# Kernel tuning notes

Measured on AMD Instinct MI355X. Metric: run time of the kernel, lower is better.

Reference implementation:

```python
import jax, jax.numpy as jnp
import numpy as np

B, N, DIN, D, E, STEP = 4, 1024, 256, 256, 5, 5


def setup_inputs() -> dict:
    key = jax.random.key(0)
    ks = jax.random.split(key, 14)
    s = 0.02  # weight init scale
    inp = {
        "node_features": jax.random.normal(ks[0], (B, N, DIN), dtype=jnp.float32),
        # dense per-edge-type adjacency; scaled so messages stay in a sane range
        "adj_matrices": jax.random.uniform(ks[1], (B, E, N, N), dtype=jnp.float32) * (2.0 / N),
        "fc_in_w": jax.random.normal(ks[2], (D, DIN), dtype=jnp.float32) * s,
        "fc_in_b": jnp.zeros((D,), dtype=jnp.float32),
        "edge_w": jax.random.normal(ks[3], (E, D, D), dtype=jnp.float32) * s,
        "edge_b": jax.random.normal(ks[4], (E, D), dtype=jnp.float32) * s,
        "gru_w_ih": jax.random.normal(ks[5], (3 * D, D), dtype=jnp.float32) * s,
        "gru_w_hh": jax.random.normal(ks[6], (3 * D, D), dtype=jnp.float32) * s,
        "gru_b_ih": jnp.zeros((3 * D,), dtype=jnp.float32),
        "gru_b_hh": jnp.zeros((3 * D,), dtype=jnp.float32),
        "conv1_w": jax.random.normal(ks[7], (D, D), dtype=jnp.float32) * s,
        "conv1_b": jnp.zeros((D,), dtype=jnp.float32),
        "conv2_w": jax.random.normal(ks[8], (D, D), dtype=jnp.float32) * s,
        "conv2_b": jnp.zeros((D,), dtype=jnp.float32),
    }
    return inp


def _gru_cell(x, h, w_ih, w_hh, b_ih, b_hh):
    # torch GRUCell: gates ordered [r, z, n]
    gi = x @ w_ih.T + b_ih  # [B*N, 3D]
    gh = h @ w_hh.T + b_hh
    ir, iz, inn = jnp.split(gi, 3, axis=-1)
    hr, hz, hn = jnp.split(gh, 3, axis=-1)
    r = jax.nn.sigmoid(ir + hr)
    z = jax.nn.sigmoid(iz + hz)
    n = jnp.tanh(inn + r * hn)
    return (1.0 - z) * n + z * h


def reference(node_features, adj_matrices, fc_in_w, fc_in_b, edge_w, edge_b,
              gru_w_ih, gru_w_hh, gru_b_ih, gru_b_hh,
              conv1_w, conv1_b, conv2_w, conv2_b):
    h = node_features @ fc_in_w.T + fc_in_b  # [B, N, D]
    sum_edge_b = jnp.sum(edge_b, axis=0)  # accumulated biases over edge types
    for _ in range(STEP):
        # messages per edge type: adj_e @ h  -> [B, E, N, D]
        msgs = jnp.einsum('benm,bmd->bend', adj_matrices, h)
        # per-edge-type linear (y = x @ W_e.T) then accumulate over edge types
        acc = jnp.einsum('bend,ekd->bnk', msgs, edge_w) + sum_edge_b  # [B, N, D]
        h = _gru_cell(acc, h, gru_w_ih, gru_w_hh, gru_b_ih, gru_b_hh)
    node_states = h  # [B, N, D]
    # conv1d with kernel_size=1 over node axis == per-node linear on channels
    attn_weights = jax.nn.sigmoid(node_states @ conv1_w.T + conv1_b)  # [B, N, D]
    feats = jnp.tanh(node_states @ conv2_w.T + conv2_b)  # [B, N, D]
    graph_embedding = jnp.sum(attn_weights * feats, axis=1)  # sum over nodes -> [B, D]
    attn_map = jnp.mean(attn_weights, axis=2)  # mean over channels -> [B, N]
    return (graph_embedding, node_states, attn_map)
```

## Files before the change

kernel.cpp:

```cpp
#include <hip/hip_runtime.h>
#include <hip/hip_bf16.h>
#include <cstdint>


typedef __attribute__((ext_vector_type(8))) short bf16x8;
typedef __attribute__((ext_vector_type(4))) float f32x4;

__device__ __forceinline__ float bf2f(__hip_bfloat16 x) { return __bfloat162float(x); }
__device__ __forceinline__ __hip_bfloat16 f2bf(float x) { return __float2bfloat16(x); }
__device__ __forceinline__ short f2bs(float x) {
  __hip_bfloat16 h = __float2bfloat16(x);
  return *reinterpret_cast<short*>(&h);
}

__device__ __forceinline__ bf16x8 ld8_ext(const void* base, long off, bool f32) {
  if (f32) {
    const float* p = (const float*)base + off;
    bf16x8 r;
#pragma unroll
    for (int i = 0; i < 8; ++i) r[i] = f2bs(p[i]);
    return r;
  }
  return *(const bf16x8*)((const __hip_bfloat16*)base + off);
}

__global__ void detect_dtype(const uint32_t* __restrict__ raw, int* __restrict__ flag) {
  __shared__ int cnt;
  if (threadIdx.x == 0) cnt = 0;
  __syncthreads();
  int c = 0;
  for (int i = threadIdx.x; i < 512; i += 256) {
    uint32_t byte = (raw[i] >> 8) & 0xFF;
    if (byte >= 0x28 && byte <= 0x40) ++c;
  }
  atomicAdd(&cnt, c);
  __syncthreads();
  if (threadIdx.x == 0) *flag = (cnt < 300) ? 1 : 0;
}

__global__ void prep_pool(const void* fcb, const void* bih, const void* bhh,
                          const void* c1b, const void* c2b, const void* edgeb,
                          const int* __restrict__ flag,
                          float* __restrict__ pool, float* __restrict__ ge) {
  const bool f32 = (*flag != 0);
  for (int t = threadIdx.x; t < 2560; t += 256) {
    const void* p; int i;
    if (t < 256)       { p = fcb;  i = t; }
    else if (t < 1024) { p = bih;  i = t - 256; }
    else if (t < 1792) { p = bhh;  i = t - 1024; }
    else if (t < 2048) { p = c1b;  i = t - 1792; }
    else if (t < 2304) { p = c2b;  i = t - 2048; }
    else {
      int k = t - 2304; float s = 0.f;
      for (int e = 0; e < 5; ++e)
        s += f32 ? ((const float*)edgeb)[e * 256 + k]
                 : bf2f(((const __hip_bfloat16*)edgeb)[e * 256 + k]);
      pool[t] = s; continue;
    }
    pool[t] = f32 ? ((const float*)p)[i] : bf2f(((const __hip_bfloat16*)p)[i]);
  }
  for (int t = threadIdx.x; t < 1024; t += 256) ge[t] = 0.f;
}

__global__ void wcvt_all(const void* fcw, const void* edw, const void* wih,
                         const void* whh, const void* c1w, const void* c2w,
                         const int* __restrict__ flag, __hip_bfloat16* __restrict__ dst) {
  const bool f32 = (*flag != 0);
  const int i = blockIdx.x * 256 + threadIdx.x;
  const void* src; int off;
  if      (i < 65536)  { src = fcw; off = i; }
  else if (i < 393216) { src = edw; off = i - 65536; }
  else if (i < 589824) { src = wih; off = i - 393216; }
  else if (i < 786432) { src = whh; off = i - 589824; }
  else if (i < 851968) { src = c1w; off = i - 786432; }
  else                 { src = c2w; off = i - 851968; }
  dst[i] = f32 ? f2bf(((const float*)src)[off])
               : ((const __hip_bfloat16*)src)[off];
}

__global__ void adj_cvt(const void* __restrict__ src, const int* __restrict__ flag,
                        __hip_bfloat16* __restrict__ dst) {
  const bool f32 = (*flag != 0);
  const long i = ((long)blockIdx.x * 256 + threadIdx.x) * 8;
  bf16x8 r;
  if (f32) {
    const float* p = (const float*)src + i;
#pragma unroll
    for (int j = 0; j < 8; ++j) r[j] = f2bs(p[j]);
  } else {
    r = *(const bf16x8*)((const __hip_bfloat16*)src + i);
  }
  *(bf16x8*)(dst + i) = r;
}

__global__ void acc_finish(const float* __restrict__ p, const float* __restrict__ pool,
                           __hip_bfloat16* __restrict__ out) {
  const long i = (long)blockIdx.x * 256 + threadIdx.x;
  const int b = (int)(i >> 18);
  const long base = (long)b * 5 * 262144 + (i & 262143);
  float s = pool[2304 + (i & 255)];
#pragma unroll
  for (int e = 0; e < 5; ++e) s += p[base + (long)e * 262144];
  out[i] = f2bf(s);
}

template<int OUT_MODE, bool HAS_BIAS, bool A_EXT, bool DUAL>
__global__ __launch_bounds__(256)
void gemm_bt(const void* __restrict__ A, const __hip_bfloat16* __restrict__ Bt,
             const float* __restrict__ bias, void* __restrict__ Cp,
             const void* __restrict__ A2, const __hip_bfloat16* __restrict__ Bt2,
             const float* __restrict__ bias2, void* __restrict__ Cp2,
             const int* __restrict__ flag,
             int Kg, int ngrp, int lda, int ldb, int ldc,
             long aBatch, int zdivA, int zmodA,
             long bBatch, int zdivB, int zmodB,
             long cBatch, int zdivC, long aGrp, long bGrp, int zSplit)
{
  __shared__ __align__(16) __hip_bfloat16 sA[64 * 64];
  __shared__ __align__(16) __hip_bfloat16 sB[64 * 64];
  const bool af32 = A_EXT ? (*flag != 0) : false;
  const int t = threadIdx.x;
  const int w = t >> 6;
  const int l = t & 63;
  const int m0 = blockIdx.x * 64;
  const int n0 = blockIdx.y * 64;
  int z = blockIdx.z;

  const void* Au = A; const __hip_bfloat16* Btu = Bt;
  const float* biasu = bias; void* Cpu = Cp;
  if (DUAL && z >= zSplit) { Au = A2; Btu = Bt2; biasu = bias2; Cpu = Cp2; z -= zSplit; }

  const long aOff = (long)((z / zdivA) % zmodA) * aBatch;
  const __hip_bfloat16* Bb = Btu + (long)((z / zdivB) % zmodB) * bBatch;

  const int p0 = t, p1 = t + 256;
  const int sr0 = p0 >> 3, sc0 = (p0 & 7) ^ (sr0 & 7);
  const int sr1 = p1 >> 3, sc1 = (p1 & 7) ^ (sr1 & 7);

  f32x4 acc[4];
#pragma unroll
  for (int i = 0; i < 4; ++i) acc[i] = (f32x4){0.f, 0.f, 0.f, 0.f};

  const int mrow = w * 16 + (l & 15);
  const int quad = l >> 4;

  for (int g = 0; g < ngrp; ++g) {
    const long aG = aOff + (long)g * aGrp;
    const __hip_bfloat16* Bg = Bb + (long)g * bGrp;
    for (int k0 = 0; k0 < Kg; k0 += 64) {
      bf16x8 a0, a1;
      if (A_EXT) {
        a0 = ld8_ext(Au, aG + (long)(m0 + sr0) * lda + (k0 + sc0 * 8), af32);
        a1 = ld8_ext(Au, aG + (long)(m0 + sr1) * lda + (k0 + sc1 * 8), af32);
      } else {
        const __hip_bfloat16* Ab = (const __hip_bfloat16*)Au;
        a0 = *(const bf16x8*)(Ab + aG + (long)(m0 + sr0) * lda + (k0 + sc0 * 8));
        a1 = *(const bf16x8*)(Ab + aG + (long)(m0 + sr1) * lda + (k0 + sc1 * 8));
      }
      bf16x8 b0 = *(const bf16x8*)(Bg + (long)(n0 + sr0) * ldb + (k0 + sc0 * 8));
      bf16x8 b1 = *(const bf16x8*)(Bg + (long)(n0 + sr1) * ldb + (k0 + sc1 * 8));
      __syncthreads();
      *(bf16x8*)(sA + p0 * 8) = a0;
      *(bf16x8*)(sA + p1 * 8) = a1;
      *(bf16x8*)(sB + p0 * 8) = b0;
      *(bf16x8*)(sB + p1 * 8) = b1;
      __syncthreads();
#pragma unroll
      for (int ks = 0; ks < 2; ++ks) {
        const int cg = ks * 4 + quad;
        bf16x8 af = *(const bf16x8*)(sA + mrow * 64 + ((cg ^ (mrow & 7)) * 8));
#pragma unroll
        for (int t4 = 0; t4 < 4; ++t4) {
          const int nrow = t4 * 16 + (l & 15);
          bf16x8 bfr = *(const bf16x8*)(sB + nrow * 64 + ((cg ^ (nrow & 7)) * 8));
          acc[t4] = __builtin_amdgcn_mfma_f32_16x16x32_bf16(af, bfr, acc[t4], 0, 0, 0);
        }
      }
    }
  }

  const long cOff = (long)(z / zdivC) * cBatch;
#pragma unroll
  for (int t4 = 0; t4 < 4; ++t4) {
    const int n = n0 + t4 * 16 + (l & 15);
    float bv = 0.f;
    if (HAS_BIAS) bv = biasu[n];
#pragma unroll
    for (int r = 0; r < 4; ++r) {
      const int m = m0 + w * 16 + quad * 4 + r;
      const float v = acc[t4][r] + bv;
      if (OUT_MODE == 0)
        ((__hip_bfloat16*)Cpu)[cOff + (long)m * ldc + n] = f2bf(v);
      else
        ((float*)Cpu)[cOff + (long)m * ldc + n] = v;
    }
  }
}

__global__ void gru_gate(const __hip_bfloat16* __restrict__ gi,
                         const __hip_bfloat16* __restrict__ gh,
                         __hip_bfloat16* __restrict__ hbf,
                         void* __restrict__ ns_out, const int* __restrict__ flag)
{
  const int m = blockIdx.x;
  const int k = threadIdx.x;
  const long gb = (long)m * 768;
  const float ir = bf2f(gi[gb + k]);
  const float iz = bf2f(gi[gb + 256 + k]);
  const float inn = bf2f(gi[gb + 512 + k]);
  const float hr = bf2f(gh[gb + k]);
  const float hz = bf2f(gh[gb + 256 + k]);
  const float hn = bf2f(gh[gb + 512 + k]);
  const long hidx = (long)m * 256 + k;
  const float h = bf2f(hbf[hidx]);
  const float r = 1.f / (1.f + __expf(-(ir + hr)));
  const float zz = 1.f / (1.f + __expf(-(iz + hz)));
  const float nn = tanhf(inn + r * hn);
  const float hnew = (1.f - zz) * nn + zz * h;
  const __hip_bfloat16 hb = f2bf(hnew);
  hbf[hidx] = hb;
  if (ns_out) {
    if (*flag) ((float*)ns_out)[1024 + hidx] = hnew;
    else       ((__hip_bfloat16*)ns_out)[1024 + hidx] = hb;
  }
}

__global__ void ge_partial(const float* __restrict__ attnl,
                           const float* __restrict__ featl,
                           float* __restrict__ ge)
{
  const int b = blockIdx.y;
  const int k = threadIdx.x;
  float gacc = 0.f;
  for (int i = 0; i < 8; ++i) {
    const int node = blockIdx.x * 8 + i;
    const long idx = ((long)b * 1024 + node) * 256 + k;
    const float a = 1.f / (1.f + __expf(-attnl[idx]));
    const float f = tanhf(featl[idx]);
    gacc += a * f;
  }
  atomicAdd(&ge[b * 256 + k], gacc);
}

__global__ void attn_map_k(const float* __restrict__ attnl,
                           void* __restrict__ dout, const int* __restrict__ flag)
{
  const int node = blockIdx.x * 4 + (threadIdx.x >> 6);
  const int l = threadIdx.x & 63;
  const float4 v = *((const float4*)attnl + (long)node * 64 + l);
  float s = 1.f / (1.f + __expf(-v.x)) + 1.f / (1.f + __expf(-v.y)) +
            1.f / (1.f + __expf(-v.z)) + 1.f / (1.f + __expf(-v.w));
  for (int off = 32; off; off >>= 1) s += __shfl_down(s, off, 64);
  if (l == 0) {
    const float am = s * (1.f / 256.f);
    if (*flag) ((float*)dout)[1049600 + node] = am;
    else       ((__hip_bfloat16*)dout)[1049600 + node] = f2bf(am);
  }
}

__global__ void ge_finish(const float* __restrict__ ge, void* __restrict__ dout,
                          const int* __restrict__ flag)
{
  const int t = blockIdx.x * 256 + threadIdx.x;
  if (*flag) ((float*)dout)[t] = ge[t];
  else       ((__hip_bfloat16*)dout)[t] = f2bf(ge[t]);
}

extern "C" void kernel_launch(void* const* d_in, const int* in_sizes, int n_in,
                              void* d_out, int out_size, void* d_ws, size_t ws_size,
                              hipStream_t stream) {
  (void)in_sizes; (void)n_in; (void)out_size;
  const void* node_f = d_in[0];
  const void* adj    = d_in[1];
  const void* fc_w   = d_in[2];
  const void* fc_b   = d_in[3];
  const void* edge_w = d_in[4];
  const void* edge_b = d_in[5];
  const void* w_ih   = d_in[6];
  const void* w_hh   = d_in[7];
  const void* b_ih   = d_in[8];
  const void* b_hh   = d_in[9];
  const void* c1w    = d_in[10];
  const void* c1b    = d_in[11];
  const void* c2w    = d_in[12];
  const void* c2b    = d_in[13];

  char* ws = (char*)d_ws;
  const size_t MB = (size_t)1 << 20;
  int*            flag = (int*)(ws);
  float*          bp   = (float*)(ws + 256);
  float*          ge   = (float*)(ws + 10496);
  __hip_bfloat16* wbf  = (__hip_bfloat16*)(ws + 14592);
  __hip_bfloat16* hbf  = (__hip_bfloat16*)(ws + 1849600);
  char*           S    = ws + 3946752;
  __hip_bfloat16* heT  = (__hip_bfloat16*)(S);
  float*          part = (float*)(S + 12 * MB);
  __hip_bfloat16* accb = (__hip_bfloat16*)(S + 32 * MB);
  __hip_bfloat16* gi   = (__hip_bfloat16*)(S);
  __hip_bfloat16* gh   = (__hip_bfloat16*)(S + 6 * MB);
  float*          attl = (float*)(S);
  float*          fetl = (float*)(S + 4 * MB);
  __hip_bfloat16* adjb = (__hip_bfloat16*)(ws + 40 * MB);

  const bool has_split = ws_size >= 40 * MB;
  const bool has_adjb  = ws_size >= 81 * MB;

  detect_dtype<<<1, 256, 0, stream>>>((const uint32_t*)adj, flag);
  prep_pool<<<1, 256, 0, stream>>>(fc_b, b_ih, b_hh, c1b, c2b, edge_b, flag, bp, ge);
  wcvt_all<<<3584, 256, 0, stream>>>(fc_w, edge_w, w_ih, w_hh, c1w, c2w, flag, wbf);
  if (has_adjb) adj_cvt<<<10240, 256, 0, stream>>>(adj, flag, adjb);

  gemm_bt<0, true, true, false><<<dim3(64, 4, 1), 256, 0, stream>>>(
      node_f, wbf + 0, bp + 0, hbf, nullptr, nullptr, nullptr, nullptr, flag,
      256, 1, 256, 256, 256, 0, 1, 1, 0, 1, 1, 0, 1, 0, 0, 0);

  for (int s = 0; s < 5; ++s) {
    gemm_bt<0, false, false, false><<<dim3(4, 16, 20), 256, 0, stream>>>(
        wbf + 65536, hbf, nullptr, heT, nullptr, nullptr, nullptr, nullptr, flag,
        256, 1, 256, 256, 1024,
        65536, 1, 5, 262144, 5, 4,
        262144, 1, 0, 0, 0);
    if (has_split) {
      if (has_adjb) {
        gemm_bt<1, false, false, false><<<dim3(16, 4, 20), 256, 0, stream>>>(
            adjb, heT, nullptr, part, nullptr, nullptr, nullptr, nullptr, flag,
            1024, 1, 1024, 1024, 256,
            1048576, 1, 20, 262144, 1, 20,
            262144, 1, 0, 0, 0);
      } else {
        gemm_bt<1, false, true, false><<<dim3(16, 4, 20), 256, 0, stream>>>(
            adj, heT, nullptr, part, nullptr, nullptr, nullptr, nullptr, flag,
            1024, 1, 1024, 1024, 256,
            1048576, 1, 20, 262144, 1, 20,
            262144, 1, 0, 0, 0);
      }
      acc_finish<<<4096, 256, 0, stream>>>(part, bp, accb);
    } else {
      gemm_bt<0, true, true, false><<<dim3(16, 4, 4), 256, 0, stream>>>(
          adj, heT, bp + 2304, accb, nullptr, nullptr, nullptr, nullptr, flag,
          1024, 5, 1024, 1024, 256,
          (long)5 * 1048576, 1, 4, (long)5 * 262144, 1, 4,
          262144, 1, 1048576, 262144, 0);
    }
    gemm_bt<0, true, false, true><<<dim3(64, 12, 2), 256, 0, stream>>>(
        accb, wbf + 393216, bp + 256, gi,
        hbf,  wbf + 589824, bp + 1024, gh, flag,
        256, 1, 256, 256, 768, 0, 1, 1, 0, 1, 1, 0, 1, 0, 0, 1);
    gru_gate<<<4096, 256, 0, stream>>>(gi, gh, hbf,
                                       (s == 4) ? d_out : nullptr, flag);
  }

  gemm_bt<1, true, false, true><<<dim3(64, 4, 2), 256, 0, stream>>>(
      hbf, wbf + 786432, bp + 1792, attl,
      hbf, wbf + 851968, bp + 2048, fetl, flag,
      256, 1, 256, 256, 256, 0, 1, 1, 0, 1, 1, 0, 1, 0, 0, 1);

  ge_partial<<<dim3(128, 4), 256, 0, stream>>>(attl, fetl, ge);
  attn_map_k<<<1024, 256, 0, stream>>>(attl, d_out, flag);
  ge_finish<<<4, 256, 0, stream>>>(ge, d_out, flag);
}
```

Baseline: 461.3 us.

## Fuse split-K reduction into GRU gemm and fuse conv heads with pooling

The split-K adjacency GEMM now writes bf16 partials, and the GRU input GEMM sums the five edge-type partials while loading its A tile. This removes the separate acc_finish pass and the fp32 partial buffer. The edge-bias contribution is folded algebraically into a precomputed gi bias (W_ih · sum_edge_b). The two conv1 GEMMs, sigmoid/tanh, graph-embedding reduction and attention-map mean are fused into one kernel using shared and global atomics, replacing four kernels and the fp32 attl/fetl intermediates. The trade-offs are lower precision in the partials and extra redundant partial reads in the GRU GEMM across its 12 N-tiles.

```diff
diff --git a/kernel.cpp b/kernel.cpp
--- a/kernel.cpp
+++ b/kernel.cpp
@@ -12,6 +12,10 @@
   __hip_bfloat16 h = __float2bfloat16(x);
   return *reinterpret_cast<short*>(&h);
 }
+__device__ __forceinline__ float s2f(short x) {
+  __hip_bfloat16 h = *reinterpret_cast<__hip_bfloat16*>(&x);
+  return __bfloat162float(h);
+}
 
 __device__ __forceinline__ bf16x8 ld8_ext(const void* base, long off, bool f32) {
   if (f32) {
@@ -22,6 +26,21 @@
     return r;
   }
   return *(const bf16x8*)((const __hip_bfloat16*)base + off);
+}
+
+__device__ __forceinline__ bf16x8 ld8_sum5(const __hip_bfloat16* part, int row, int k) {
+  const long base = (long)row * 256 + (long)(row >> 10) * 1048576 + k;
+  float s[8] = {0.f, 0.f, 0.f, 0.f, 0.f, 0.f, 0.f, 0.f};
+#pragma unroll
+  for (int e = 0; e < 5; ++e) {
+    bf16x8 v = *(const bf16x8*)(part + base + e * 262144);
+#pragma unroll
+    for (int j = 0; j < 8; ++j) s[j] += s2f(v[j]);
+  }
+  bf16x8 r;
+#pragma unroll
+  for (int j = 0; j < 8; ++j) r[j] = f2bs(s[j]);
+  return r;
 }
 
 __global__ void detect_dtype(const uint32_t* __restrict__ raw, int* __restrict__ flag) {
@@ -41,7 +60,8 @@
 __global__ void prep_pool(const void* fcb, const void* bih, const void* bhh,
                           const void* c1b, const void* c2b, const void* edgeb,
                           const int* __restrict__ flag,
-                          float* __restrict__ pool, float* __restrict__ ge) {
+                          float* __restrict__ pool, float* __restrict__ ge,
+                          float* __restrict__ am32) {
   const bool f32 = (*flag != 0);
   for (int t = threadIdx.x; t < 2560; t += 256) {
     const void* p; int i;
@@ -60,6 +80,17 @@
     pool[t] = f32 ? ((const float*)p)[i] : bf2f(((const __hip_bfloat16*)p)[i]);
   }
   for (int t = threadIdx.x; t < 1024; t += 256) ge[t] = 0.f;
+  for (int t = threadIdx.x; t < 4096; t += 256) am32[t] = 0.f;
+}
+
+__global__ void bias_gi_k(const float* __restrict__ pool,
+                          const __hip_bfloat16* __restrict__ wih,
+                          float* __restrict__ out) {
+  const int n = blockIdx.x * 256 + threadIdx.x;
+  if (n >= 768) return;
+  float s = pool[256 + n];
+  for (int k = 0; k < 256; ++k) s += pool[2304 + k] * bf2f(wih[n * 256 + k]);
+  out[n] = s;
 }
 
 __global__ void wcvt_all(const void* fcw, const void* edw, const void* wih,
@@ -93,18 +124,7 @@
   *(bf16x8*)(dst + i) = r;
 }
 
-__global__ void acc_finish(const float* __restrict__ p, const float* __restrict__ pool,
-                           __hip_bfloat16* __restrict__ out) {
-  const long i = (long)blockIdx.x * 256 + threadIdx.x;
-  const int b = (int)(i >> 18);
-  const long base = (long)b * 5 * 262144 + (i & 262143);
-  float s = pool[2304 + (i & 255)];
-#pragma unroll
-  for (int e = 0; e < 5; ++e) s += p[base + (long)e * 262144];
-  out[i] = f2bf(s);
-}
-
-template<int OUT_MODE, bool HAS_BIAS, bool A_EXT, bool DUAL>
+template<int OUT_MODE, bool HAS_BIAS, int A_MODE, bool DUAL>
 __global__ __launch_bounds__(256)
 void gemm_bt(const void* __restrict__ A, const __hip_bfloat16* __restrict__ Bt,
              const float* __restrict__ bias, void* __restrict__ Cp,
@@ -118,7 +138,7 @@
 {
   __shared__ __align__(16) __hip_bfloat16 sA[64 * 64];
   __shared__ __align__(16) __hip_bfloat16 sB[64 * 64];
-  const bool af32 = A_EXT ? (*flag != 0) : false;
+  const bool af32 = (A_MODE == 1) ? (*flag != 0) : false;
   const int t = threadIdx.x;
   const int w = t >> 6;
   const int l = t & 63;
@@ -128,7 +148,10 @@
 
   const void* Au = A; const __hip_bfloat16* Btu = Bt;
   const float* biasu = bias; void* Cpu = Cp;
-  if (DUAL && z >= zSplit) { Au = A2; Btu = Bt2; biasu = bias2; Cpu = Cp2; z -= zSplit; }
+  bool second = false;
+  if (DUAL && z >= zSplit) {
+    Au = A2; Btu = Bt2; biasu = bias2; Cpu = Cp2; z -= zSplit; second = true;
+  }
 
   const long aOff = (long)((z / zdivA) % zmodA) * aBatch;
   const __hip_bfloat16* Bb = Btu + (long)((z / zdivB) % zmodB) * bBatch;
@@ -149,7 +172,10 @@
     const __hip_bfloat16* Bg = Bb + (long)g * bGrp;
     for (int k0 = 0; k0 < Kg; k0 += 64) {
       bf16x8 a0, a1;
-      if (A_EXT) {
+      if (A_MODE == 2 && !second) {
+        a0 = ld8_sum5((const __hip_bfloat16*)Au, m0 + sr0, k0 + sc0 * 8);
+        a1 = ld8_sum5((const __hip_bfloat16*)Au, m0 + sr1, k0 + sc1 * 8);
+      } else if (A_MODE == 1) {
         a0 = ld8_ext(Au, aG + (long)(m0 + sr0) * lda + (k0 + sc0 * 8), af32);
         a1 = ld8_ext(Au, aG + (long)(m0 + sr1) * lda + (k0 + sc1 * 8), af32);
       } else {
@@ -225,45 +251,90 @@
   }
 }
 
-__global__ void ge_partial(const float* __restrict__ attnl,
-                           const float* __restrict__ featl,
-                           float* __restrict__ ge)
+__global__ __launch_bounds__(256)
+void conv_fused(const __hip_bfloat16* __restrict__ hbf,
+                const __hip_bfloat16* __restrict__ c1w,
+                const __hip_bfloat16* __restrict__ c2w,
+                const float* __restrict__ pool,
+                float* __restrict__ geg, float* __restrict__ am32)
 {
-  const int b = blockIdx.y;
-  const int k = threadIdx.x;
-  float gacc = 0.f;
-  for (int i = 0; i < 8; ++i) {
-    const int node = blockIdx.x * 8 + i;
-    const long idx = ((long)b * 1024 + node) * 256 + k;
-    const float a = 1.f / (1.f + __expf(-attnl[idx]));
-    const float f = tanhf(featl[idx]);
-    gacc += a * f;
-  }
-  atomicAdd(&ge[b * 256 + k], gacc);
-}
-
-__global__ void attn_map_k(const float* __restrict__ attnl,
+  __shared__ __align__(16) __hip_bfloat16 sA[64 * 64];
+  __shared__ __align__(16) __hip_bfloat16 sB1[64 * 64];
+  __shared__ __align__(16) __hip_bfloat16 sB2[64 * 64];
+  __shared__ float sge[64];
+  __shared__ float sam[64];
+  const int t = threadIdx.x, w = t >> 6, l = t & 63;
+  const int m0 = blockIdx.x * 64, n0 = blockIdx.y * 64;
+  if (t < 64) { sge[t] = 0.f; sam[t] = 0.f; }
+  const int p0 = t, p1 = t + 256;
+  const int sr0 = p0 >> 3, sc0 = (p0 & 7) ^ (sr0 & 7);
+  const int sr1 = p1 >> 3, sc1 = (p1 & 7) ^ (sr1 & 7);
+  f32x4 a1[4], a2[4];
+#pragma unroll
+  for (int i = 0; i < 4; ++i) { a1[i] = (f32x4){0,0,0,0}; a2[i] = (f32x4){0,0,0,0}; }
+  const int mrow = w * 16 + (l & 15);
+  const int quad = l >> 4;
+  for (int k0 = 0; k0 < 256; k0 += 64) {
+    bf16x8 va0 = *(const bf16x8*)(hbf + (long)(m0 + sr0) * 256 + (k0 + sc0 * 8));
+    bf16x8 va1 = *(const bf16x8*)(hbf + (long)(m0 + sr1) * 256 + (k0 + sc1 * 8));
+    bf16x8 vb0 = *(const bf16x8*)(c1w + (long)(n0 + sr0) * 256 + (k0 + sc0 * 8));
+    bf16x8 vb1 = *(const bf16x8*)(c1w + (long)(n0 + sr1) * 256 + (k0 + sc1 * 8));
+    bf16x8 vc0 = *(const bf16x8*)(c2w + (long)(n0 + sr0) * 256 + (k0 + sc0 * 8));
+    bf16x8 vc1 = *(const bf16x8*)(c2w + (long)(n0 + sr1) * 256 + (k0 + sc1 * 8));
+    __syncthreads();
+    *(bf16x8*)(sA + p0 * 8) = va0;  *(bf16x8*)(sA + p1 * 8) = va1;
+    *(bf16x8*)(sB1 + p0 * 8) = vb0; *(bf16x8*)(sB1 + p1 * 8) = vb1;
+    *(bf16x8*)(sB2 + p0 * 8) = vc0; *(bf16x8*)(sB2 + p1 * 8) = vc1;
+    __syncthreads();
+#pragma unroll
+    for (int ks = 0; ks < 2; ++ks) {
+      const int cg = ks * 4 + quad;
+      bf16x8 af = *(const bf16x8*)(sA + mrow * 64 + ((cg ^ (mrow & 7)) * 8));
+#pragma unroll
+      for (int t4 = 0; t4 < 4; ++t4) {
+        const int nrow = t4 * 16 + (l & 15);
+        bf16x8 b1f = *(const bf16x8*)(sB1 + nrow * 64 + ((cg ^ (nrow & 7)) * 8));
+        bf16x8 b2f = *(const bf16x8*)(sB2 + nrow * 64 + ((cg ^ (nrow & 7)) * 8));
+        a1[t4] = __builtin_amdgcn_mfma_f32_16x16x32_bf16(af, b1f, a1[t4], 0, 0, 0);
+        a2[t4] = __builtin_amdgcn_mfma_f32_16x16x32_bf16(af, b2f, a2[t4], 0, 0, 0);
+      }
+    }
+  }
+  float asum[4] = {0.f, 0.f, 0.f, 0.f};
+#pragma unroll
+  for (int t4 = 0; t4 < 4; ++t4) {
+    const int n = n0 + t4 * 16 + (l & 15);
+    const float bb1 = pool[1792 + n], bb2 = pool[2048 + n];
+    float g = 0.f;
+#pragma unroll
+    for (int r = 0; r < 4; ++r) {
+      const float av = 1.f / (1.f + __expf(-(a1[t4][r] + bb1)));
+      const float fv = tanhf(a2[t4][r] + bb2);
+      g += av * fv;
+      asum[r] += av;
+    }
+    atomicAdd(&sge[t4 * 16 + (l & 15)], g);
+  }
+#pragma unroll
+  for (int r = 0; r < 4; ++r) atomicAdd(&sam[w * 16 + quad * 4 + r], asum[r]);
+  __syncthreads();
+  if (t < 64) atomicAdd(&geg[(m0 >> 10) * 256 + n0 + t], sge[t]);
+  else if (t < 128) atomicAdd(&am32[m0 + (t - 64)], sam[t - 64]);
+}
+
+__global__ void finish_out(const float* __restrict__ ge, const float* __restrict__ am32,
                            void* __restrict__ dout, const int* __restrict__ flag)
 {
-  const int node = blockIdx.x * 4 + (threadIdx.x >> 6);
-  const int l = threadIdx.x & 63;
-  const float4 v = *((const float4*)attnl + (long)node * 64 + l);
-  float s = 1.f / (1.f + __expf(-v.x)) + 1.f / (1.f + __expf(-v.y)) +
-            1.f / (1.f + __expf(-v.z)) + 1.f / (1.f + __expf(-v.w));
-  for (int off = 32; off; off >>= 1) s += __shfl_down(s, off, 64);
-  if (l == 0) {
-    const float am = s * (1.f / 256.f);
-    if (*flag) ((float*)dout)[1049600 + node] = am;
-    else       ((__hip_bfloat16*)dout)[1049600 + node] = f2bf(am);
-  }
-}
-
-__global__ void ge_finish(const float* __restrict__ ge, void* __restrict__ dout,
-                          const int* __restrict__ flag)
-{
   const int t = blockIdx.x * 256 + threadIdx.x;
-  if (*flag) ((float*)dout)[t] = ge[t];
-  else       ((__hip_bfloat16*)dout)[t] = f2bf(ge[t]);
+  const bool f32 = (*flag != 0);
+  if (t < 1024) {
+    if (f32) ((float*)dout)[t] = ge[t];
+    else     ((__hip_bfloat16*)dout)[t] = f2bf(ge[t]);
+  } else {
+    const float v = am32[t - 1024] * (1.f / 256.f);
+    if (f32) ((float*)dout)[1049600 + t - 1024] = v;
+    else     ((__hip_bfloat16*)dout)[1049600 + t - 1024] = f2bf(v);
+  }
 }
 
 extern "C" void kernel_launch(void* const* d_in, const int* in_sizes, int n_in,
@@ -289,73 +360,70 @@
   const size_t MB = (size_t)1 << 20;
   int*            flag = (int*)(ws);
   float*          bp   = (float*)(ws + 256);
-  float*          ge   = (float*)(ws + 10496);
-  __hip_bfloat16* wbf  = (__hip_bfloat16*)(ws + 14592);
-  __hip_bfloat16* hbf  = (__hip_bfloat16*)(ws + 1849600);
-  char*           S    = ws + 3946752;
+  float*          ge   = (float*)(ws + 14336);
+  float*          am32 = (float*)(ws + 18432);
+  __hip_bfloat16* wbf  = (__hip_bfloat16*)(ws + 34816);
+  __hip_bfloat16* hbf  = (__hip_bfloat16*)(ws + 1869824);
+  char*           S    = ws + 3966976;
   __hip_bfloat16* heT  = (__hip_bfloat16*)(S);
-  float*          part = (float*)(S + 12 * MB);
-  __hip_bfloat16* accb = (__hip_bfloat16*)(S + 32 * MB);
-  __hip_bfloat16* gi   = (__hip_bfloat16*)(S);
-  __hip_bfloat16* gh   = (__hip_bfloat16*)(S + 6 * MB);
-  float*          attl = (float*)(S);
-  float*          fetl = (float*)(S + 4 * MB);
+  __hip_bfloat16* part = (__hip_bfloat16*)(S + 10 * MB);
+  __hip_bfloat16* gi   = (__hip_bfloat16*)(S + 20 * MB);
+  __hip_bfloat16* gh   = (__hip_bfloat16*)(S + 26 * MB);
   __hip_bfloat16* adjb = (__hip_bfloat16*)(ws + 40 * MB);
 
-  const bool has_split = ws_size >= 40 * MB;
+  const bool has_split = ws_size >= 38 * MB;
   const bool has_adjb  = ws_size >= 81 * MB;
 
   detect_dtype<<<1, 256, 0, stream>>>((const uint32_t*)adj, flag);
-  prep_pool<<<1, 256, 0, stream>>>(fc_b, b_ih, b_hh, c1b, c2b, edge_b, flag, bp, ge);
+  prep_pool<<<1, 256, 0, stream>>>(fc_b, b_ih, b_hh, c1b, c2b, edge_b, flag, bp, ge, am32);
   wcvt_all<<<3584, 256, 0, stream>>>(fc_w, edge_w, w_ih, w_hh, c1w, c2w, flag, wbf);
+  bias_gi_k<<<3, 256, 0, stream>>>(bp, wbf + 393216, bp + 2560);
   if (has_adjb) adj_cvt<<<10240, 256, 0, stream>>>(adj, flag, adjb);
 
-  gemm_bt<0, true, true, false><<<dim3(64, 4, 1), 256, 0, stream>>>(
+  gemm_bt<0, true, 1, false><<<dim3(64, 4, 1), 256, 0, stream>>>(
       node_f, wbf + 0, bp + 0, hbf, nullptr, nullptr, nullptr, nullptr, flag,
       256, 1, 256, 256, 256, 0, 1, 1, 0, 1, 1, 0, 1, 0, 0, 0);
 
   for (int s = 0; s < 5; ++s) {
-    gemm_bt<0, false, false, false><<<dim3(4, 16, 20), 256, 0, stream>>>(
+    gemm_bt<0, false, 0, false><<<dim3(4, 16, 20), 256, 0, stream>>>(
         wbf + 65536, hbf, nullptr, heT, nullptr, nullptr, nullptr, nullptr, flag,
         256, 1, 256, 256, 1024,
         65536, 1, 5, 262144, 5, 4,
         262144, 1, 0, 0, 0);
     if (has_split) {
       if (has_adjb) {
-        gemm_bt<1, false, false, false><<<dim3(16, 4, 20), 256, 0, stream>>>(
+        gemm_bt<0, false, 0, false><<<dim3(16, 4, 20), 256, 0, stream>>>(
             adjb, heT, nullptr, part, nullptr, nullptr, nullptr, nullptr, flag,
             1024, 1, 1024, 1024, 256,
             1048576, 1, 20, 262144, 1, 20,
             262144, 1, 0, 0, 0);
       } else {
-        gemm_bt<1, false, true, false><<<dim3(16, 4, 20), 256, 0, stream>>>(
+        gemm_bt<0, false, 1, false><<<dim3(16, 4, 20), 256, 0, stream>>>(
             adj, heT, nullptr, part, nullptr, nullptr, nullptr, nullptr, flag,
             1024, 1, 1024, 1024, 256,
             1048576, 1, 20, 262144, 1, 20,
             262144, 1, 0, 0, 0);
       }
-      acc_finish<<<4096, 256, 0, stream>>>(part, bp, accb);
+      gemm_bt<0, true, 2, true><<<dim3(64, 12, 2), 256, 0, stream>>>(
+          part, wbf + 393216, bp + 2560, gi,
+          hbf,  wbf + 589824, bp + 1024, gh, flag,
+          256, 1, 256, 256, 768, 0, 1, 1, 0, 1, 1, 0, 1, 0, 0, 1);
     } else {
-      gemm_bt<0, true, true, false><<<dim3(16, 4, 4), 256, 0, stream>>>(
-          adj, heT, bp + 2304, accb, nullptr, nullptr, nullptr, nullptr, flag,
+      gemm_bt<0, true, 1, false><<<dim3(16, 4, 4), 256, 0, stream>>>(
+          adj, heT, bp + 2304, part, nullptr, nullptr, nullptr, nullptr, flag,
           1024, 5, 1024, 1024, 256,
           (long)5 * 1048576, 1, 4, (long)5 * 262144, 1, 4,
           262144, 1, 1048576, 262144, 0);
-    }
-    gemm_bt<0, true, false, true><<<dim3(64, 12, 2), 256, 0, stream>>>(
-        accb, wbf + 393216, bp + 256, gi,
-        hbf,  wbf + 589824, bp + 1024, gh, flag,
-        256, 1, 256, 256, 768, 0, 1, 1, 0, 1, 1, 0, 1, 0, 0, 1);
+      gemm_bt<0, true, 0, true><<<dim3(64, 12, 2), 256, 0, stream>>>(
+          part, wbf + 393216, bp + 256, gi,
+          hbf,  wbf + 589824, bp + 1024, gh, flag,
+          256, 1, 256, 256, 768, 0, 1, 1, 0, 1, 1, 0, 1, 0, 0, 1);
+    }
     gru_gate<<<4096, 256, 0, stream>>>(gi, gh, hbf,
                                        (s == 4) ? d_out : nullptr, flag);
   }
 
-  gemm_bt<1, true, false, true><<<dim3(64, 4, 2), 256, 0, stream>>>(
-      hbf, wbf + 786432, bp + 1792, attl,
-      hbf, wbf + 851968, bp + 2048, fetl, flag,
-      256, 1, 256, 256, 256, 0, 1, 1, 0, 1, 1, 0, 1, 0, 0, 1);
-
-  ge_partial<<<dim3(128, 4), 256, 0, stream>>>(attl, fetl, ge);
-  attn_map_k<<<1024, 256, 0, stream>>>(attl, d_out, flag);
-  ge_finish<<<4, 256, 0, stream>>>(ge, d_out, flag);
-}
+  conv_fused<<<dim3(64, 4), 256, 0, stream>>>(hbf, wbf + 786432, wbf + 851968,
+                                              bp, ge, am32);
+  finish_out<<<20, 256, 0, stream>>>(ge, am32, d_out, flag);
+}
```

Result: no change. 453.9 us (-1.6%).
